# Kernel optimization log

Measured on AMD Instinct MI355X. Metric: run time of the kernel, lower is better.

## Reference

```python
import jax, jax.numpy as jnp
import numpy as np

VOCAB, D, H = 32000, 1024, 16
DH = D // H
DFF = 4 * D
EPS = 1e-5


def layer_norm(x, g, b):
    mu = jnp.mean(x, axis=-1, keepdims=True)
    var = jnp.var(x, axis=-1, keepdims=True)
    return (x - mu) * jax.lax.rsqrt(var + EPS) * g + b


def pos_enc(seq_len, d_model):
    # faithful to the torch double-loop: angle = pos / 10000**(2*i/d) for even index i
    pos = jnp.arange(seq_len, dtype=jnp.float32)[:, None]          # [S,1]
    i_even = jnp.arange(0, d_model, 2, dtype=jnp.float32)[None, :]  # [1,D/2]
    angle = pos / jnp.power(10000.0, 2.0 * i_even / d_model)        # [S,D/2]
    pe = jnp.zeros((seq_len, d_model), dtype=jnp.float32)
    pe = pe.at[:, 0::2].set(jnp.sin(angle))
    pe = pe.at[:, 1::2].set(jnp.cos(angle))
    return pe


def setup_inputs() -> dict:
    key = jax.random.key(0)
    ks = jax.random.split(key, 16)
    s = 0.02
    return {
        "tokens": jax.random.randint(ks[0], (4, 2048), 0, VOCAB),
        "emb": jax.random.normal(ks[1], (VOCAB, D), jnp.float32) * s,
        "in_proj_w": jax.random.normal(ks[2], (3 * D, D), jnp.float32) * s,
        "in_proj_b": jnp.zeros((3 * D,), jnp.float32),
        "out_proj_w": jax.random.normal(ks[3], (D, D), jnp.float32) * s,
        "out_proj_b": jnp.zeros((D,), jnp.float32),
        "w1": jax.random.normal(ks[4], (DFF, D), jnp.float32) * s,
        "b1": jnp.zeros((DFF,), jnp.float32),
        "w2": jax.random.normal(ks[5], (D, DFF), jnp.float32) * s,
        "b2": jnp.zeros((D,), jnp.float32),
        "g1": jnp.ones((D,), jnp.float32),
        "beta1": jnp.zeros((D,), jnp.float32),
        "g2": jnp.ones((D,), jnp.float32),
        "beta2": jnp.zeros((D,), jnp.float32),
    }


def reference(tokens, emb, in_proj_w, in_proj_b, out_proj_w, out_proj_b,
              w1, b1, w2, b2, g1, beta1, g2, beta2):
    B, S = tokens.shape
    x = emb[tokens] + pos_enc(S, D)[None, :, :]                 # [B,S,D]
    # multi-head self-attention (eval mode, no dropout)
    qkv = x @ in_proj_w.T + in_proj_b                           # [B,S,3D]
    q, k, v = jnp.split(qkv, 3, axis=-1)
    q = q.reshape(B, S, H, DH)
    k = k.reshape(B, S, H, DH)
    v = v.reshape(B, S, H, DH)
    scores = jnp.einsum("bqhd,bkhd->bhqk", q, k) / jnp.sqrt(jnp.float32(DH))
    attn = jax.nn.softmax(scores, axis=-1)
    ctx = jnp.einsum("bhqk,bkhd->bqhd", attn, v).reshape(B, S, D)
    attn_out = ctx @ out_proj_w.T + out_proj_b
    h = layer_norm(x + attn_out, g1, beta1)
    ff = jax.nn.relu(h @ w1.T + b1) @ w2.T + b2
    return layer_norm(h + ff, g2, beta2)
```

## Files before the change

kernel.cpp:

```cpp
#include <hip/hip_runtime.h>
#include <math.h>

#define DMODEL 1024
#define NH 16
#define DHEAD 64
#define DFF 4096
#define BATCH 4
#define SEQ 2048
#define MROWS (BATCH * SEQ)
#define LNEPS 1e-5f
#define NT (SEQ / 64)

typedef __attribute__((ext_vector_type(8))) short bf16x8;
typedef __attribute__((ext_vector_type(4))) float f32x4;
typedef __attribute__((ext_vector_type(16))) float f32x16;
typedef __attribute__((ext_vector_type(4))) unsigned int u32x4;

__device__ inline unsigned short f2bf(float f) {
  unsigned int u = __float_as_uint(f);
  unsigned int r = (u + 0x7fffu + ((u >> 16) & 1u)) >> 16;
  return (unsigned short)r;
}

__device__ inline void gload16(const unsigned short* g, char* l) {
  __builtin_amdgcn_global_load_lds(
      (const __attribute__((address_space(1))) unsigned int*)g,
      (__attribute__((address_space(3))) unsigned int*)l, 16, 0, 0);
}

__device__ inline float fexp2(float x) {
  float r;
  asm("v_exp_f32 %0, %1" : "=v"(r) : "v"(x));
  return r;
}
__device__ inline unsigned int cvtpk(float lo, float hi) {
  unsigned int r;
  asm("v_cvt_pk_bf16_f32 %0, %1, %2" : "=v"(r) : "v"(lo), "v"(hi));
  return r;
}
__device__ inline void plswap(unsigned int& a, unsigned int& b) {
  asm("v_permlane32_swap_b32 %0, %1" : "+v"(a), "+v"(b));
}

__global__ __launch_bounds__(256)
void embed_kernel(const int* __restrict__ tokens, const float* __restrict__ emb,
                  float* __restrict__ X, unsigned short* __restrict__ Xb) {
  const int HALF = DMODEL / 2;
  int idx = blockIdx.x * 256 + threadIdx.x;
  if (idx >= MROWS * HALF) return;
  int row = idx / HALF;
  int j = idx - row * HALF;
  int s = row & (SEQ - 1);
  int tok = tokens[row];
  float2 e = ((const float2*)(emb + (size_t)tok * DMODEL))[j];
  float denom = powf(10000.0f, (2.0f * (float)(2 * j)) / (float)DMODEL);
  float ang = (float)s / denom;
  float sn, cs;
  sincosf(ang, &sn, &cs);
  float2 o;
  o.x = e.x + sn;
  o.y = e.y + cs;
  ((float2*)(X + (size_t)row * DMODEL))[j] = o;
  ushort2 ob;
  ob.x = f2bf(o.x); ob.y = f2bf(o.y);
  ((ushort2*)(Xb + (size_t)row * DMODEL))[j] = ob;
}

__global__ __launch_bounds__(256)
void cvt4_kernel(const float* __restrict__ a, const float* __restrict__ b,
                 const float* __restrict__ c, const float* __restrict__ d,
                 unsigned short* __restrict__ oa, unsigned short* __restrict__ ob,
                 unsigned short* __restrict__ oc, unsigned short* __restrict__ od) {
  int i = blockIdx.x * 256 + threadIdx.x;
  const float* src; unsigned short* dst; int off;
  if (i < 786432)       { src = a; dst = oa; off = 0; }
  else if (i < 1048576) { src = b; dst = ob; off = 786432; }
  else if (i < 2097152) { src = c; dst = oc; off = 1048576; }
  else                  { src = d; dst = od; off = 2097152; }
  int j = i - off;
  float4 v = ((const float4*)src)[j];
  ushort4 o;
  o.x = f2bf(v.x); o.y = f2bf(v.y); o.z = f2bf(v.z); o.w = f2bf(v.w);
  ((ushort4*)dst)[j] = o;
}

__device__ inline void stage256(const unsigned short* G, char* base, int row0,
                                int K, int kt, int t) {
#pragma unroll
  for (int i = 0; i < 4; ++i) {
    int g = i * 512 + t;
    int row = g >> 3, sl = g & 7;
    int c = sl ^ (row & 7);
    gload16(G + (size_t)(row0 + row) * K + kt * 64 + c * 8, base + g * 16);
  }
}

__global__ __launch_bounds__(512, 2)
void gemm256(const unsigned short* __restrict__ A, const unsigned short* __restrict__ B,
             const float* __restrict__ bias, const float* __restrict__ resid,
             float* __restrict__ Cf, unsigned short* __restrict__ Cb,
             int M, int N, int K, int relu) {
  extern __shared__ char smem[];

  const int t = threadIdx.x;
  const int lane = t & 63;
  const int wv = t >> 6;
  const int wm = wv >> 2;
  const int wn = wv & 3;
  const int fr = lane & 15;
  const int fq = lane >> 4;

  const int nwg = gridDim.x;
  const int orig = blockIdx.x;
  const int q8 = nwg >> 3;
  const int wgid = (orig & 7) * q8 + (orig >> 3);
  const int stid = wgid >> 2, within = wgid & 3;
  const int sm = within & 1, sn = within >> 1;
  const int Msup = M >> 9;
  const int stm = stid % Msup, stn = stid / Msup;
  const int m0 = (stm * 2 + sm) * 256;
  const int n0 = (stn * 2 + sn) * 256;

  f32x4 acc[8][4];
#pragma unroll
  for (int m = 0; m < 8; ++m)
#pragma unroll
    for (int n = 0; n < 4; ++n) acc[m][n] = (f32x4){0.f, 0.f, 0.f, 0.f};

  const int nk = K / 64;

  stage256(A, smem, m0, K, 0, t);
  stage256(B, smem + 32768, n0, K, 0, t);

  for (int kt = 0; kt < nk; ++kt) {
    const int buf = kt & 1;
    asm volatile("s_waitcnt vmcnt(0)" ::: "memory");
    __builtin_amdgcn_s_barrier();
    if (kt + 1 < nk) {
      char* nxt = smem + ((buf ^ 1) << 16);
      stage256(A, nxt, m0, K, kt + 1, t);
      stage256(B, nxt + 32768, n0, K, kt + 1, t);
    }
    const unsigned short* Al = (const unsigned short*)(smem + (buf << 16));
    const unsigned short* Bl = (const unsigned short*)(smem + (buf << 16) + 32768);

    bf16x8 bfr[4][2];
#pragma unroll
    for (int n = 0; n < 4; ++n) {
      int brow = wn * 64 + n * 16 + fr;
#pragma unroll
      for (int ks = 0; ks < 2; ++ks)
        bfr[n][ks] = *(const bf16x8*)&Bl[brow * 64 + (((ks * 4 + fq) ^ (brow & 7)) * 8)];
    }
#pragma unroll
    for (int mp = 0; mp < 4; ++mp) {
      bf16x8 af[2][2];
#pragma unroll
      for (int mm = 0; mm < 2; ++mm) {
        int arow = wm * 128 + (mp * 2 + mm) * 16 + fr;
#pragma unroll
        for (int ks = 0; ks < 2; ++ks)
          af[mm][ks] = *(const bf16x8*)&Al[arow * 64 + (((ks * 4 + fq) ^ (arow & 7)) * 8)];
      }
      __builtin_amdgcn_s_setprio(1);
#pragma unroll
      for (int mm = 0; mm < 2; ++mm)
#pragma unroll
        for (int n = 0; n < 4; ++n)
#pragma unroll
          for (int ks = 0; ks < 2; ++ks)
            acc[mp * 2 + mm][n] = __builtin_amdgcn_mfma_f32_16x16x32_bf16(
                af[mm][ks], bfr[n][ks], acc[mp * 2 + mm][n], 0, 0, 0);
      __builtin_amdgcn_s_setprio(0);
    }
  }

  float* slab = (float*)(smem + wv * 4352);
#pragma unroll
  for (int m = 0; m < 8; ++m) {
#pragma unroll
    for (int n = 0; n < 4; ++n)
#pragma unroll
      for (int j = 0; j < 4; ++j)
        slab[(fq * 4 + j) * 68 + n * 16 + fr] = acc[m][n][j];
    int rg0 = m0 + wm * 128 + m * 16;
#pragma unroll
    for (int it = 0; it < 4; ++it) {
      int u = it * 64 + lane;
      int row = u >> 4, seg = u & 15;
      float4 v = *(const float4*)&slab[row * 68 + seg * 4];
      int col = n0 + wn * 64 + seg * 4;
      float4 b4 = *(const float4*)&bias[col];
      v.x += b4.x; v.y += b4.y; v.z += b4.z; v.w += b4.w;
      if (relu) {
        v.x = fmaxf(v.x, 0.f); v.y = fmaxf(v.y, 0.f);
        v.z = fmaxf(v.z, 0.f); v.w = fmaxf(v.w, 0.f);
      }
      size_t idx = (size_t)(rg0 + row) * N + col;
      if (resid) {
        float4 r4 = *(const float4*)&resid[idx];
        v.x += r4.x; v.y += r4.y; v.z += r4.z; v.w += r4.w;
      }
      if (Cf) {
        *(float4*)&Cf[idx] = v;
      } else {
        ushort4 ob;
        ob.x = f2bf(v.x); ob.y = f2bf(v.y); ob.z = f2bf(v.z); ob.w = f2bf(v.w);
        *(ushort4*)&Cb[idx] = ob;
      }
    }
  }
}

#define AOFF(buf) ((buf) * 49152)
#define BOFF(buf) ((buf) * 49152 + 32768)

__device__ inline void stageA(const unsigned short* Ag, char* smem_, int buf,
                              int m0, int K, int kt, int wv, int lane) {
  int rl = lane >> 3, c = (lane & 7) ^ rl;
#pragma unroll
  for (int i = 0; i < 4; ++i) {
    int r0 = (wv * 4 + i) * 8;
    gload16(Ag + (size_t)(m0 + r0 + rl) * K + kt * 64 + c * 8,
            smem_ + AOFF(buf) + r0 * 128 + lane * 16);
  }
}
__device__ inline void stageB2(const unsigned short* Bg, char* smem_, int buf,
                               int n0, int K, int kt, int wv, int lane) {
  int rl = lane >> 3, c = (lane & 7) ^ rl;
#pragma unroll
  for (int i = 0; i < 2; ++i) {
    int r0 = (wv * 2 + i) * 8;
    gload16(Bg + (size_t)(n0 + r0 + rl) * K + kt * 64 + c * 8,
            smem_ + BOFF(buf) + r0 * 128 + lane * 16);
  }
}

#define VM6 asm volatile("s_waitcnt vmcnt(6)" ::: "memory")
#define VM0 asm volatile("s_waitcnt vmcnt(0)" ::: "memory")

#define DO_PHASE(buf, mb, LOADB, STAGE_STMT, WAIT_STMT)                         \
  {                                                                             \
    bf16x8 af[2][2];                                                            \
    _Pragma("unroll") for (int mm = 0; mm < 2; ++mm) {                          \
      int arow = wm * 64 + ((mb) + mm) * 16 + fr;                               \
      _Pragma("unroll") for (int ks = 0; ks < 2; ++ks) {                        \
        int slot = (ks * 4 + fq) ^ (arow & 7);                                  \
        af[mm][ks] = *(const bf16x8*)(smem + AOFF(buf) + arow * 128 + slot * 16); \
      }                                                                         \
    }                                                                           \
    if (LOADB) {                                                                \
      _Pragma("unroll") for (int n = 0; n < 4; ++n) {                           \
        int brow = wn * 64 + n * 16 + fr;                                       \
        _Pragma("unroll") for (int ks = 0; ks < 2; ++ks) {                      \
          int slot = (ks * 4 + fq) ^ (brow & 7);                                \
          bfr[n][ks] = *(const bf16x8*)(smem + BOFF(buf) + brow * 128 + slot * 16); \
        }                                                                       \
      }                                                                         \
    }                                                                           \
    STAGE_STMT;                                                                 \
    __builtin_amdgcn_sched_barrier(0);                                          \
    __builtin_amdgcn_s_barrier();                                               \
    __builtin_amdgcn_sched_barrier(0);                                          \
    __builtin_amdgcn_s_setprio(1);                                              \
    _Pragma("unroll") for (int mm = 0; mm < 2; ++mm)                            \
      _Pragma("unroll") for (int n = 0; n < 4; ++n)                             \
        _Pragma("unroll") for (int ks = 0; ks < 2; ++ks)                        \
          acc[(mb) + mm][n] = __builtin_amdgcn_mfma_f32_16x16x32_bf16(          \
              af[mm][ks], bfr[n][ks], acc[(mb) + mm][n], 0, 0, 0);              \
    __builtin_amdgcn_s_setprio(0);                                              \
    WAIT_STMT;                                                                  \
    __builtin_amdgcn_sched_barrier(0);                                          \
    __builtin_amdgcn_s_barrier();                                               \
    __builtin_amdgcn_sched_barrier(0);                                          \
  }

__global__ __launch_bounds__(512, 2)
void gemm8(const unsigned short* __restrict__ A, const unsigned short* __restrict__ B,
           const float* __restrict__ bias, const float* __restrict__ resid,
           float* __restrict__ Cf, unsigned short* __restrict__ Cb,
           int M, int N, int K, int relu) {
  extern __shared__ char smem[];

  const int t = threadIdx.x;
  const int lane = t & 63;
  const int wv = t >> 6;
  const int wm = wv >> 1;
  const int wn = wv & 1;
  const int fr = lane & 15;
  const int fq = lane >> 4;

  const int nwg = gridDim.x;
  const int orig = blockIdx.x;
  const int q8 = nwg >> 3;
  const int wgid = (orig & 7) * q8 + (orig >> 3);
  const int stid = wgid >> 4, within = wgid & 15;
  const int sm = within & 3, sn = within >> 2;
  const int Msup = M >> 10;
  const int stm = stid % Msup, stn = stid / Msup;
  const int m0 = (stm * 4 + sm) * 256;
  const int n0 = (stn * 4 + sn) * 128;

  f32x4 acc[4][4];
#pragma unroll
  for (int m = 0; m < 4; ++m)
#pragma unroll
    for (int n = 0; n < 4; ++n) acc[m][n] = (f32x4){0.f, 0.f, 0.f, 0.f};

  const int nk = K / 64;
  const int nj = nk / 2;

  stageB2(B, smem, 0, n0, K, 0, wv, lane);
  stageA (A, smem, 0, m0, K, 0, wv, lane);
  stageB2(B, smem, 1, n0, K, 1, wv, lane);
  stageA (A, smem, 1, m0, K, 1, wv, lane);
  VM6;
  __builtin_amdgcn_sched_barrier(0);
  __builtin_amdgcn_s_barrier();
  __builtin_amdgcn_sched_barrier(0);

  for (int j = 0; j < nj - 1; ++j) {
    const int k0 = 2 * j, k1 = 2 * j + 1;
    const int s0k = k0 + 2, s1k = k1 + 2;
    const int b0 = k0 % 3, b1 = k1 % 3;
    const int sb0 = s0k % 3, sb1 = s1k % 3;
    bf16x8 bfr[4][2];
    DO_PHASE(b0, 0, true,  stageB2(B, smem, sb0, n0, K, s0k, wv, lane), );
    DO_PHASE(b0, 2, false, stageA (A, smem, sb0, m0, K, s0k, wv, lane), VM6);
    DO_PHASE(b1, 0, true,  stageB2(B, smem, sb1, n0, K, s1k, wv, lane), );
    DO_PHASE(b1, 2, false, stageA (A, smem, sb1, m0, K, s1k, wv, lane), VM6);
  }
  {
    const int b0 = (nk - 2) % 3, b1 = (nk - 1) % 3;
    bf16x8 bfr[4][2];
    DO_PHASE(b0, 0, true,  , );
    DO_PHASE(b0, 2, false, , VM0);
    DO_PHASE(b1, 0, true,  , );
    DO_PHASE(b1, 2, false, , );
  }

  float* slab = (float*)(smem + wv * 4352);
#pragma unroll
  for (int m = 0; m < 4; ++m) {
#pragma unroll
    for (int n = 0; n < 4; ++n)
#pragma unroll
      for (int j = 0; j < 4; ++j)
        slab[(fq * 4 + j) * 68 + n * 16 + fr] = acc[m][n][j];
    int rg0 = m0 + wm * 64 + m * 16;
#pragma unroll
    for (int it = 0; it < 4; ++it) {
      int u = it * 64 + lane;
      int row = u >> 4, seg = u & 15;
      float4 v = *(const float4*)&slab[row * 68 + seg * 4];
      int col = n0 + wn * 64 + seg * 4;
      float4 b4 = *(const float4*)&bias[col];
      v.x += b4.x; v.y += b4.y; v.z += b4.z; v.w += b4.w;
      if (relu) {
        v.x = fmaxf(v.x, 0.f); v.y = fmaxf(v.y, 0.f);
        v.z = fmaxf(v.z, 0.f); v.w = fmaxf(v.w, 0.f);
      }
      size_t idx = (size_t)(rg0 + row) * N + col;
      if (resid) {
        float4 r4 = *(const float4*)&resid[idx];
        v.x += r4.x; v.y += r4.y; v.z += r4.z; v.w += r4.w;
      }
      if (Cf) {
        *(float4*)&Cf[idx] = v;
      } else {
        ushort4 ob;
        ob.x = f2bf(v.x); ob.y = f2bf(v.y); ob.z = f2bf(v.z); ob.w = f2bf(v.w);
        *(ushort4*)&Cb[idx] = ob;
      }
    }
  }
}

__global__ __launch_bounds__(256)
void vtrans_kernel(const unsigned short* __restrict__ qkvb, unsigned short* __restrict__ vtb) {
  __shared__ __align__(16) unsigned short tile[64][64];
  const int st = blockIdx.x;
  const int bh = blockIdx.y;
  const int b = bh >> 4, h = bh & 15;
  const int t = threadIdx.x;
#pragma unroll
  for (int p = 0; p < 2; ++p) {
    int item = p * 256 + t;
    int r = item >> 3, c8 = item & 7;
    const unsigned short* src =
        qkvb + (size_t)(b * SEQ + st * 64 + r) * (3 * DMODEL) + 2048 + h * 64 + c8 * 8;
    *(uint4*)&tile[r][(c8 ^ (r & 7)) * 8] = *(const uint4*)src;
  }
  __syncthreads();
#pragma unroll
  for (int p = 0; p < 2; ++p) {
    int item = p * 256 + t;
    int d = item & 63, s8 = item >> 6;
    unsigned short v[8];
#pragma unroll
    for (int e = 0; e < 8; ++e) {
      int s = s8 * 8 + e;
      v[e] = tile[s][(((d >> 3) ^ (s & 7)) * 8) + (d & 7)];
    }
    uint4 u;
    u.x = (unsigned int)v[0] | ((unsigned int)v[1] << 16);
    u.y = (unsigned int)v[2] | ((unsigned int)v[3] << 16);
    u.z = (unsigned int)v[4] | ((unsigned int)v[5] << 16);
    u.w = (unsigned int)v[6] | ((unsigned int)v[7] << 16);
    *(uint4*)(vtb + ((size_t)bh * 64 + d) * SEQ + st * 64 + s8 * 8) = u;
  }
}

__global__ __launch_bounds__(512, 4)
void attn_kernel(const unsigned short* __restrict__ qkv, const unsigned short* __restrict__ vtb,
                 unsigned short* __restrict__ ctxb) {
  __shared__ __align__(16) unsigned short Ks[2][64][64];
  __shared__ __align__(16) unsigned short Vts[2][64][64];
  __shared__ __align__(16) unsigned short Slab[8][32][64];

  const int t = threadIdx.x;
  const int lane = t & 63;
  const int wq = t >> 6;
  const int l31 = lane & 31;
  const int hi1 = lane >> 5;
  const int bid = blockIdx.x;
  const int bh = bid & 63;
  const int qt = bid >> 6;
  const int b = bh >> 4, h = bh & 15;
  const int q0 = qt * 256;

  const size_t RS = 3 * DMODEL;
  const unsigned short* qb = qkv + (size_t)b * SEQ * RS + h * DHEAD;
  const unsigned short* kb = qb + DMODEL;

  bf16x8 qf[4];
  {
    const unsigned short* qrow = qb + (size_t)(q0 + wq * 32 + l31) * RS;
#pragma unroll
    for (int s = 0; s < 4; ++s)
      qf[s] = *(const bf16x8*)(qrow + s * 16 + hi1 * 8);
  }

  const unsigned short* kgl =
      kb + (size_t)(wq * 8 + (lane >> 3)) * RS + ((lane & 7) ^ (lane >> 3)) * 8;
  const unsigned short* vgl =
      vtb + ((size_t)bh * 64 + wq * 8 + (lane >> 3)) * SEQ + ((lane & 7) ^ (lane >> 3)) * 8;

  f32x16 oacc[2] = {};
  float lacc = 0.f;

  gload16(kgl, (char*)&Ks[0][wq * 8][0]);
  gload16(vgl, (char*)&Vts[0][wq * 8][0]);
  __syncthreads();

  const float C = 0.18033688011112042f;

  for (int kt = 0; kt < NT; ++kt) {
    const int cur = kt & 1;
    if (kt + 1 < NT) {
      gload16(kgl + (size_t)(kt + 1) * 64 * RS, (char*)&Ks[cur ^ 1][wq * 8][0]);
      gload16(vgl + (size_t)(kt + 1) * 64, (char*)&Vts[cur ^ 1][wq * 8][0]);
    }

    f32x16 sacc[2] = {};
    __builtin_amdgcn_s_setprio(1);
#pragma unroll
    for (int s = 0; s < 4; ++s) {
#pragma unroll
      for (int kvt = 0; kvt < 2; ++kvt) {
        int row = kvt * 32 + l31;
        bf16x8 kf = *(const bf16x8*)&Ks[cur][row][(((2 * s + hi1) ^ (row & 7)) * 8)];
        sacc[kvt] = __builtin_amdgcn_mfma_f32_32x32x16_bf16(kf, qf[s], sacc[kvt], 0, 0, 0);
      }
    }
    __builtin_amdgcn_s_setprio(0);

#pragma unroll
    for (int kvt = 0; kvt < 2; ++kvt) {
      float p[16];
#pragma unroll
      for (int r = 0; r < 16; ++r) p[r] = fexp2(sacc[kvt][r] * C);
      float ps = 0.f;
#pragma unroll
      for (int r = 0; r < 16; ++r) ps += p[r];
      lacc += ps;
#pragma unroll
      for (int half = 0; half < 2; ++half) {
        const int lo = half * 8;
        unsigned int x0 = cvtpk(p[lo + 0], p[lo + 1]);
        unsigned int x1 = cvtpk(p[lo + 2], p[lo + 3]);
        unsigned int y0 = cvtpk(p[lo + 4], p[lo + 5]);
        unsigned int y1 = cvtpk(p[lo + 6], p[lo + 7]);
        plswap(x0, y0);
        plswap(x1, y1);
        bf16x8 pa = __builtin_bit_cast(bf16x8, (u32x4){x0, x1, y0, y1});
        const int s2 = kvt * 2 + half;
        __builtin_amdgcn_s_setprio(1);
#pragma unroll
        for (int dt = 0; dt < 2; ++dt) {
          int vrow = dt * 32 + l31;
          bf16x8 vf = *(const bf16x8*)&Vts[cur][vrow][(((2 * s2 + hi1) ^ (vrow & 7)) * 8)];
          oacc[dt] = __builtin_amdgcn_mfma_f32_32x32x16_bf16(pa, vf, oacc[dt], 0, 0, 0);
        }
        __builtin_amdgcn_s_setprio(0);
      }
    }
    __syncthreads();
  }

  lacc += __shfl_xor(lacc, 32);
  float inv = 1.0f / lacc;

  float iv[16];
#pragma unroll
  for (int r = 0; r < 16; ++r)
    iv[r] = __shfl(inv, (r & 3) + 8 * (r >> 2) + 4 * hi1);

#pragma unroll
  for (int dt = 0; dt < 2; ++dt) {
    const int chunk = dt * 4 + (l31 >> 3);
    const int e7 = l31 & 7;
#pragma unroll
    for (int r = 0; r < 16; ++r) {
      int qp = (r & 3) + 8 * (r >> 2) + 4 * hi1;
      Slab[wq][qp][((chunk ^ (qp & 7)) * 8) + e7] = f2bf(oacc[dt][r] * iv[r]);
    }
  }
#pragma unroll
  for (int it = 0; it < 4; ++it) {
    int u = it * 64 + lane;
    int row = u >> 3, s = u & 7;
    uint4 v = *(const uint4*)&Slab[wq][row][((s ^ (row & 7)) * 8)];
    *(uint4*)(ctxb + (size_t)(b * SEQ + q0 + wq * 32 + row) * DMODEL + h * DHEAD + s * 8) = v;
  }
}

__global__ __launch_bounds__(256)
void ln_kernel(const float* __restrict__ Z, const float* __restrict__ g,
               const float* __restrict__ bta, float* __restrict__ Y,
               unsigned short* __restrict__ Yb) {
  const int row = blockIdx.x;
  const float4* z4 = (const float4*)(Z + (size_t)row * DMODEL);
  float4 v = z4[threadIdx.x];
  float s = v.x + v.y + v.z + v.w;
  float ss = fmaf(v.x, v.x, fmaf(v.y, v.y, fmaf(v.z, v.z, v.w * v.w)));
#pragma unroll
  for (int o = 32; o >= 1; o >>= 1) {
    s += __shfl_xor(s, o);
    ss += __shfl_xor(ss, o);
  }
  __shared__ float red[8];
  int w = threadIdx.x >> 6;
  if ((threadIdx.x & 63) == 0) { red[w] = s; red[4 + w] = ss; }
  __syncthreads();
  s = red[0] + red[1] + red[2] + red[3];
  ss = red[4] + red[5] + red[6] + red[7];
  float mu = s * (1.0f / DMODEL);
  float var = ss * (1.0f / DMODEL) - mu * mu;
  float rs = rsqrtf(var + LNEPS);
  float4 gg = ((const float4*)g)[threadIdx.x];
  float4 bb = ((const float4*)bta)[threadIdx.x];
  float4 o;
  o.x = (v.x - mu) * rs * gg.x + bb.x;
  o.y = (v.y - mu) * rs * gg.y + bb.y;
  o.z = (v.z - mu) * rs * gg.z + bb.z;
  o.w = (v.w - mu) * rs * gg.w + bb.w;
  ((float4*)(Y + (size_t)row * DMODEL))[threadIdx.x] = o;
  if (Yb) {
    ushort4 ob;
    ob.x = f2bf(o.x); ob.y = f2bf(o.y); ob.z = f2bf(o.z); ob.w = f2bf(o.w);
    ((ushort4*)(Yb + (size_t)row * DMODEL))[threadIdx.x] = ob;
  }
}

extern "C" void kernel_launch(void* const* d_in, const int* in_sizes, int n_in,
                              void* d_out, int out_size, void* d_ws, size_t ws_size,
                              hipStream_t stream) {
  const int* tokens       = (const int*)d_in[0];
  const float* emb        = (const float*)d_in[1];
  const float* in_proj_w  = (const float*)d_in[2];
  const float* in_proj_b  = (const float*)d_in[3];
  const float* out_proj_w = (const float*)d_in[4];
  const float* out_proj_b = (const float*)d_in[5];
  const float* w1         = (const float*)d_in[6];
  const float* b1         = (const float*)d_in[7];
  const float* w2         = (const float*)d_in[8];
  const float* b2         = (const float*)d_in[9];
  const float* g1         = (const float*)d_in[10];
  const float* beta1      = (const float*)d_in[11];
  const float* g2         = (const float*)d_in[12];
  const float* beta2      = (const float*)d_in[13];
  float* out = (float*)d_out;

  char* ws = (char*)d_ws;
  const size_t MB = 1ull << 20;
  unsigned short* inwb  = (unsigned short*)(ws + 0 * MB);
  unsigned short* outwb = (unsigned short*)(ws + 6 * MB);
  unsigned short* w1b   = (unsigned short*)(ws + 8 * MB);
  unsigned short* w2b   = (unsigned short*)(ws + 16 * MB);
  float* x              = (float*)(ws + 24 * MB);
  unsigned short* xb    = (unsigned short*)(ws + 56 * MB);
  unsigned short* qkvb  = (unsigned short*)(ws + 72 * MB);
  unsigned short* vtb   = (unsigned short*)(ws + 120 * MB);
  unsigned short* ctxb  = (unsigned short*)(ws + 56 * MB);
  float* h              = (float*)(ws + 72 * MB);
  unsigned short* hb    = (unsigned short*)(ws + 104 * MB);
  unsigned short* ffbb  = (unsigned short*)(ws + 120 * MB);
  float* y2             = (float*)(ws + 24 * MB);

  const size_t GLDS8 = 147456;
  const size_t GLDS256 = 131072;

  embed_kernel<<<(MROWS * (DMODEL / 2) + 255) / 256, 256, 0, stream>>>(tokens, emb, x, xb);
  cvt4_kernel<<<12288, 256, 0, stream>>>(in_proj_w, out_proj_w, w1, w2,
                                         inwb, outwb, w1b, w2b);
  gemm256<<<(MROWS / 256) * (3 * DMODEL / 256), 512, GLDS256, stream>>>(
      xb, inwb, in_proj_b, nullptr, nullptr, qkvb, MROWS, 3 * DMODEL, DMODEL, 0);
  vtrans_kernel<<<dim3(SEQ / 64, BATCH * NH), 256, 0, stream>>>(qkvb, vtb);
  attn_kernel<<<(SEQ / 256) * (BATCH * NH), 512, 0, stream>>>(qkvb, vtb, ctxb);
  gemm8<<<(MROWS / 256) * (DMODEL / 128), 512, GLDS8, stream>>>(
      ctxb, outwb, out_proj_b, x, h, nullptr, MROWS, DMODEL, DMODEL, 0);
  ln_kernel<<<MROWS, 256, 0, stream>>>(h, g1, beta1, h, hb);
  gemm256<<<(MROWS / 256) * (DFF / 256), 512, GLDS256, stream>>>(
      hb, w1b, b1, nullptr, nullptr, ffbb, MROWS, DFF, DMODEL, 1);
  gemm8<<<(MROWS / 256) * (DMODEL / 128), 512, GLDS8, stream>>>(
      ffbb, w2b, b2, h, y2, nullptr, MROWS, DMODEL, DFF, 0);
  ln_kernel<<<MROWS, 256, 0, stream>>>(y2, g2, beta2, out, nullptr);
}
```

Before: 413.6 us.

## Rewrite 256x256 GEMM main loop as 8-phase pipelined schedule with half-tile staging

Replaces the simple double-buffered K loop of the 256x256 GEMM, used for the QKV and FFN1 projections, with an 8-phase schedule per pair of K tiles. Each phase issues a half-tile global-to-LDS load, loads fragments, and runs a quarter of the MFMAs between barriers. Partial vmcnt waits keep loads in flight across phases. The goal is to overlap global loads and LDS reads with MFMA work instead of stalling at each tile. It adds many more barriers per tile and depends on correct buffer-reuse ordering.

```diff
diff --git a/kernel.cpp b/kernel.cpp
--- a/kernel.cpp
+++ b/kernel.cpp
@@ -84,22 +84,65 @@
   ((ushort4*)dst)[j] = o;
 }
 
-__device__ inline void stage256(const unsigned short* G, char* base, int row0,
-                                int K, int kt, int t) {
-#pragma unroll
-  for (int i = 0; i < 4; ++i) {
+__device__ inline void sthalf8(const unsigned short* G, int grow0, int K, int kt,
+                               char* smem_, int isB, int half, int t) {
+  char* dst = smem_ + ((kt & 1) * 65536) + isB * 32768 + half * 16384;
+#pragma unroll
+  for (int i = 0; i < 2; ++i) {
     int g = i * 512 + t;
-    int row = g >> 3, sl = g & 7;
-    int c = sl ^ (row & 7);
-    gload16(G + (size_t)(row0 + row) * K + kt * 64 + c * 8, base + g * 16);
-  }
-}
+    int r = g >> 3, sl = g & 7;
+    int c = sl ^ (r & 7);
+    gload16(G + (size_t)(grow0 + half * 128 + r) * K + kt * 64 + c * 8, dst + g * 16);
+  }
+}
+
+#define VM4_ asm volatile("s_waitcnt vmcnt(4)" ::: "memory")
+#define VM0_ asm volatile("s_waitcnt vmcnt(0)" ::: "memory")
+
+#define PHASE8(bufofs, MG, NP, LA, LB, STAGE_STMT, WAIT_STMT)                   \
+  {                                                                             \
+    if (LA) {                                                                   \
+      _Pragma("unroll") for (int m = 0; m < 4; ++m) {                           \
+        int arow = wm * 128 + (MG) * 64 + m * 16 + fr;                          \
+        _Pragma("unroll") for (int ks = 0; ks < 2; ++ks)                        \
+          af[m][ks] = *(const bf16x8*)(smem + (bufofs) + arow * 128 +           \
+                        (((ks * 4 + fq) ^ (arow & 7)) * 16));                   \
+      }                                                                         \
+    }                                                                           \
+    if (LB) {                                                                   \
+      _Pragma("unroll") for (int nn = 0; nn < 2; ++nn) {                        \
+        int n = (NP) * 2 + nn;                                                  \
+        int brow = wn * 64 + n * 16 + fr;                                       \
+        _Pragma("unroll") for (int ks = 0; ks < 2; ++ks)                        \
+          bf[(NP) * 2 + nn][ks] = *(const bf16x8*)(smem + (bufofs) + 32768 +    \
+                        brow * 128 + (((ks * 4 + fq) ^ (brow & 7)) * 16));      \
+      }                                                                         \
+    }                                                                           \
+    STAGE_STMT;                                                                 \
+    __builtin_amdgcn_sched_barrier(0);                                          \
+    __builtin_amdgcn_s_barrier();                                               \
+    asm volatile("s_waitcnt lgkmcnt(0)" ::: "memory");                          \
+    __builtin_amdgcn_sched_barrier(0);                                          \
+    __builtin_amdgcn_s_setprio(1);                                              \
+    _Pragma("unroll") for (int m = 0; m < 4; ++m)                               \
+      _Pragma("unroll") for (int nn = 0; nn < 2; ++nn)                          \
+        _Pragma("unroll") for (int ks = 0; ks < 2; ++ks)                        \
+          acc[(MG) * 4 + m][(NP) * 2 + nn] =                                    \
+              __builtin_amdgcn_mfma_f32_16x16x32_bf16(                          \
+                  af[m][ks], bf[(NP) * 2 + nn][ks],                             \
+                  acc[(MG) * 4 + m][(NP) * 2 + nn], 0, 0, 0);                   \
+    __builtin_amdgcn_s_setprio(0);                                              \
+    WAIT_STMT;                                                                  \
+    __builtin_amdgcn_sched_barrier(0);                                          \
+    __builtin_amdgcn_s_barrier();                                               \
+    __builtin_amdgcn_sched_barrier(0);                                          \
+  }
 
 __global__ __launch_bounds__(512, 2)
-void gemm256(const unsigned short* __restrict__ A, const unsigned short* __restrict__ B,
-             const float* __restrict__ bias, const float* __restrict__ resid,
-             float* __restrict__ Cf, unsigned short* __restrict__ Cb,
-             int M, int N, int K, int relu) {
+void gemm8p(const unsigned short* __restrict__ A, const unsigned short* __restrict__ B,
+            const float* __restrict__ bias, const float* __restrict__ resid,
+            float* __restrict__ Cf, unsigned short* __restrict__ Cb,
+            int M, int N, int K, int relu) {
   extern __shared__ char smem[];
 
   const int t = threadIdx.x;
@@ -128,51 +171,40 @@
     for (int n = 0; n < 4; ++n) acc[m][n] = (f32x4){0.f, 0.f, 0.f, 0.f};
 
   const int nk = K / 64;
-
-  stage256(A, smem, m0, K, 0, t);
-  stage256(B, smem + 32768, n0, K, 0, t);
-
-  for (int kt = 0; kt < nk; ++kt) {
-    const int buf = kt & 1;
-    asm volatile("s_waitcnt vmcnt(0)" ::: "memory");
-    __builtin_amdgcn_s_barrier();
-    if (kt + 1 < nk) {
-      char* nxt = smem + ((buf ^ 1) << 16);
-      stage256(A, nxt, m0, K, kt + 1, t);
-      stage256(B, nxt + 32768, n0, K, kt + 1, t);
-    }
-    const unsigned short* Al = (const unsigned short*)(smem + (buf << 16));
-    const unsigned short* Bl = (const unsigned short*)(smem + (buf << 16) + 32768);
-
-    bf16x8 bfr[4][2];
-#pragma unroll
-    for (int n = 0; n < 4; ++n) {
-      int brow = wn * 64 + n * 16 + fr;
-#pragma unroll
-      for (int ks = 0; ks < 2; ++ks)
-        bfr[n][ks] = *(const bf16x8*)&Bl[brow * 64 + (((ks * 4 + fq) ^ (brow & 7)) * 8)];
-    }
-#pragma unroll
-    for (int mp = 0; mp < 4; ++mp) {
-      bf16x8 af[2][2];
-#pragma unroll
-      for (int mm = 0; mm < 2; ++mm) {
-        int arow = wm * 128 + (mp * 2 + mm) * 16 + fr;
-#pragma unroll
-        for (int ks = 0; ks < 2; ++ks)
-          af[mm][ks] = *(const bf16x8*)&Al[arow * 64 + (((ks * 4 + fq) ^ (arow & 7)) * 8)];
-      }
-      __builtin_amdgcn_s_setprio(1);
-#pragma unroll
-      for (int mm = 0; mm < 2; ++mm)
-#pragma unroll
-        for (int n = 0; n < 4; ++n)
-#pragma unroll
-          for (int ks = 0; ks < 2; ++ks)
-            acc[mp * 2 + mm][n] = __builtin_amdgcn_mfma_f32_16x16x32_bf16(
-                af[mm][ks], bfr[n][ks], acc[mp * 2 + mm][n], 0, 0, 0);
-      __builtin_amdgcn_s_setprio(0);
-    }
+  const int nj = nk / 2;
+
+  sthalf8(A, m0, K, 0, smem, 0, 0, t);
+  sthalf8(A, m0, K, 0, smem, 0, 1, t);
+  sthalf8(B, n0, K, 0, smem, 1, 0, t);
+  sthalf8(B, n0, K, 0, smem, 1, 1, t);
+  sthalf8(B, n0, K, 1, smem, 1, 0, t);
+  sthalf8(B, n0, K, 1, smem, 1, 1, t);
+  VM4_;
+  __builtin_amdgcn_sched_barrier(0);
+  __builtin_amdgcn_s_barrier();
+  __builtin_amdgcn_sched_barrier(0);
+
+  bf16x8 af[4][2];
+  bf16x8 bf[4][2];
+
+  for (int j = 0; j < nj; ++j) {
+    const bool st = (j + 1 < nj);
+    PHASE8(0, 0, 0, 1, 1, sthalf8(A, m0, K, 2 * j + 1, smem, 0, 0, t), );
+    PHASE8(0, 0, 1, 0, 1, sthalf8(A, m0, K, 2 * j + 1, smem, 0, 1, t), );
+    PHASE8(0, 1, 1, 1, 0,
+           if (st) sthalf8(B, n0, K, 2 * j + 2, smem, 1, 0, t), );
+    PHASE8(0, 1, 0, 0, 0,
+           if (st) sthalf8(B, n0, K, 2 * j + 2, smem, 1, 1, t),
+           { if (st) { VM4_; } else { VM0_; } });
+    PHASE8(65536, 0, 0, 1, 1,
+           if (st) sthalf8(A, m0, K, 2 * j + 2, smem, 0, 0, t), );
+    PHASE8(65536, 0, 1, 0, 1,
+           if (st) sthalf8(A, m0, K, 2 * j + 2, smem, 0, 1, t), );
+    PHASE8(65536, 1, 1, 1, 0,
+           if (st) sthalf8(B, n0, K, 2 * j + 3, smem, 1, 0, t), );
+    PHASE8(65536, 1, 0, 0, 0,
+           if (st) sthalf8(B, n0, K, 2 * j + 3, smem, 1, 1, t),
+           { if (st) { VM4_; } });
   }
 
   float* slab = (float*)(smem + wv * 4352);
@@ -609,19 +641,19 @@
   float* y2             = (float*)(ws + 24 * MB);
 
   const size_t GLDS8 = 147456;
-  const size_t GLDS256 = 131072;
+  const size_t GLDSP = 131072;
 
   embed_kernel<<<(MROWS * (DMODEL / 2) + 255) / 256, 256, 0, stream>>>(tokens, emb, x, xb);
   cvt4_kernel<<<12288, 256, 0, stream>>>(in_proj_w, out_proj_w, w1, w2,
                                          inwb, outwb, w1b, w2b);
-  gemm256<<<(MROWS / 256) * (3 * DMODEL / 256), 512, GLDS256, stream>>>(
+  gemm8p<<<(MROWS / 256) * (3 * DMODEL / 256), 512, GLDSP, stream>>>(
       xb, inwb, in_proj_b, nullptr, nullptr, qkvb, MROWS, 3 * DMODEL, DMODEL, 0);
   vtrans_kernel<<<dim3(SEQ / 64, BATCH * NH), 256, 0, stream>>>(qkvb, vtb);
   attn_kernel<<<(SEQ / 256) * (BATCH * NH), 512, 0, stream>>>(qkvb, vtb, ctxb);
   gemm8<<<(MROWS / 256) * (DMODEL / 128), 512, GLDS8, stream>>>(
       ctxb, outwb, out_proj_b, x, h, nullptr, MROWS, DMODEL, DMODEL, 0);
   ln_kernel<<<MROWS, 256, 0, stream>>>(h, g1, beta1, h, hb);
-  gemm256<<<(MROWS / 256) * (DFF / 256), 512, GLDS256, stream>>>(
+  gemm8p<<<(MROWS / 256) * (DFF / 256), 512, GLDSP, stream>>>(
       hb, w1b, b1, nullptr, nullptr, ffbb, MROWS, DFF, DMODEL, 1);
   gemm8<<<(MROWS / 256) * (DMODEL / 128), 512, GLDS8, stream>>>(
       ffbb, w2b, b2, h, y2, nullptr, MROWS, DMODEL, DFF, 0);
```

New measurement: 400.9 us. -3.1%, faster.
